# Performance work log

Measured on AMD Instinct MI355X. Metric: run time of the kernel, lower is better.

Reference implementation:

```python
import jax, jax.numpy as jnp
import numpy as np

N, IN_DIM, OUT_DIM = 8192, 512, 256

def setup_inputs() -> dict:
    key = jax.random.key(0)
    k1, k2, k3, k4, k5 = jax.random.split(key, 5)
    feat = jax.random.normal(k1, (N, IN_DIM), dtype=jnp.float32)
    counting_attn = jax.random.uniform(k2, (N, N), dtype=jnp.float32)
    Wq = jax.random.normal(k3, (IN_DIM, OUT_DIM), dtype=jnp.float32) * (IN_DIM ** -0.5)
    Wk = jax.random.normal(k4, (IN_DIM, OUT_DIM), dtype=jnp.float32) * (IN_DIM ** -0.5)
    Wv = jax.random.normal(k5, (IN_DIM, OUT_DIM), dtype=jnp.float32) * (IN_DIM ** -0.5)
    return {"feat": feat, "counting_attn": counting_attn, "Wq": Wq, "Wk": Wk, "Wv": Wv}

def reference(feat, counting_attn, Wq, Wk, Wv):
    # eval mode: feat_drop / attn_drop are identity
    Q = feat @ Wq  # [N, D]
    K = feat @ Wk
    V = feat @ Wv
    scale = 1.0 / jnp.sqrt(jnp.float32(Q.shape[1]))
    logits = (Q @ K.T) * scale  # [N, N]
    logits = logits - jnp.max(logits, axis=1, keepdims=True)
    a_nomi = jnp.exp(logits) * counting_attn
    a_deno = jnp.sum(a_nomi, axis=1, keepdims=True)
    a_nor = a_nomi / (a_deno + 1e-9)
    ret = a_nor @ V  # [N, D]
    return jax.nn.elu(ret)
```

## Files before the change

### kernel.cpp

```cpp
#include <hip/hip_runtime.h>

typedef unsigned short u16;
typedef unsigned int u32;
typedef __attribute__((ext_vector_type(8))) __bf16 bf16x8;
typedef __attribute__((ext_vector_type(16))) float f32x16;

#define NN 8192
#define IND 512
#define DD 256
#define LN_K 0.00195122595f

__device__ __forceinline__ void gl_lds16(const void* g, void* l) {
  __builtin_amdgcn_global_load_lds((const __attribute__((address_space(1))) void*)g,
                                   (__attribute__((address_space(3))) void*)l, 16, 0, 0);
}
__device__ __forceinline__ u16 bf16_rne(float x) {
  u32 u = __float_as_uint(x);
  u += 0x7FFF + ((u >> 16) & 1);
  return (u16)(u >> 16);
}

__global__ __launch_bounds__(256) void wt_transpose(const float* __restrict__ Wq,
                                                    const float* __restrict__ Wk,
                                                    const float* __restrict__ Wv,
                                                    u16* __restrict__ WT) {
  const int o = blockIdx.y;
  const int e = blockIdx.x * 256 + threadIdx.x;
  const int n = e >> 9, k = e & 511;
  const float* W = (o == 0) ? Wq : ((o == 1) ? Wk : Wv);
  WT[o * (DD * IND) + e] = bf16_rne(W[k * DD + n]);
}

__global__ __launch_bounds__(256) void cvt_feat(const float* __restrict__ f,
                                                u16* __restrict__ fb) {
  const int i = (blockIdx.x * 256 + threadIdx.x) * 4;
  float4 v = *(const float4*)(f + i);
  u32 lo = (u32)bf16_rne(v.x) | ((u32)bf16_rne(v.y) << 16);
  u32 hi = (u32)bf16_rne(v.z) | ((u32)bf16_rne(v.w) << 16);
  *(uint2*)(fb + i) = make_uint2(lo, hi);
}

__global__ __launch_bounds__(256, 2) void proj_qkv(const u16* __restrict__ featb,
                                                   const u16* __restrict__ WT,
                                                   u16* __restrict__ Qs,
                                                   u16* __restrict__ Ks,
                                                   u16* __restrict__ VTs) {
  __shared__ u16 tl[4][32 * 40];
  const int mb = blockIdx.x, o = blockIdx.y;
  const int wave = threadIdx.x >> 6, lane = threadIdx.x & 63;
  const int mm = lane & 31, h = lane >> 5;
  const int m0 = mb * 128 + wave * 32;
  const u16* wt = WT + o * (DD * IND);

  f32x16 acc[8];
#pragma unroll
  for (int nt = 0; nt < 8; ++nt)
#pragma unroll
    for (int r = 0; r < 16; ++r) acc[nt][r] = 0.f;

  for (int kc = 0; kc < 32; ++kc) {
    bf16x8 af = *(const bf16x8*)(featb + (size_t)(m0 + mm) * IND + kc * 16 + 8 * h);
#pragma unroll
    for (int nt = 0; nt < 8; ++nt) {
      bf16x8 bf = *(const bf16x8*)(wt + (size_t)(nt * 32 + mm) * IND + kc * 16 + 8 * h);
      acc[nt] = __builtin_amdgcn_mfma_f32_32x32x16_bf16(af, bf, acc[nt], 0, 0, 0);
    }
  }

  if (o < 2) {
    const float sc = (o == 0) ? 0.0625f : 1.f;
    u16* dst = (o == 0) ? Qs : Ks;
#pragma unroll
    for (int nt = 0; nt < 8; ++nt)
#pragma unroll
      for (int r = 0; r < 16; ++r) {
        const int mrow = (r & 3) + 8 * (r >> 2) + 4 * h;
        dst[(size_t)(m0 + mrow) * DD + nt * 32 + mm] = bf16_rne(acc[nt][r] * sc);
      }
  } else {
    const int n2 = lane >> 1, mh = lane & 1;
    for (int nt = 0; nt < 8; ++nt) {
#pragma unroll
      for (int r = 0; r < 16; r += 2) {
        const int mrow = (r & 3) + 8 * (r >> 2) + 4 * h;
        u32 pk = (u32)bf16_rne(acc[nt][r]) | ((u32)bf16_rne(acc[nt][r + 1]) << 16);
        *(u32*)(&tl[wave][mm * 40 + mrow]) = pk;
      }
      __syncthreads();
      bf16x8 t0 = *(const bf16x8*)(&tl[wave][n2 * 40 + mh * 16]);
      bf16x8 t1 = *(const bf16x8*)(&tl[wave][n2 * 40 + mh * 16 + 8]);
      u16* gp = VTs + (size_t)(nt * 32 + n2) * NN + m0 + mh * 16;
      *(bf16x8*)(gp) = t0;
      *(bf16x8*)(gp + 8) = t1;
      __syncthreads();
    }
  }
}

__global__ __launch_bounds__(256, 2) void flash_attn(const u16* __restrict__ Qs,
                                                     const u16* __restrict__ Ks,
                                                     const u16* __restrict__ VTs,
                                                     const float* __restrict__ cnt,
                                                     float* __restrict__ ml,
                                                     float* __restrict__ Op,
                                                     int jiters, int spl) {
  __shared__ u16 kl[2][8192];
  __shared__ u16 vl[2][8192];
  const int bid = blockIdx.x;
  const int lg = __ffs(spl) - 1;
  const int sp = bid & (spl - 1);
  const int rb = bid >> lg;
  const int wave = threadIdx.x >> 6, lane = threadIdx.x & 63;
  const int mm = lane & 31, h = lane >> 5;
  const int m0 = rb * 128 + wave * 32;
  const int jbase = sp * jiters * 32;

  bf16x8 qf[16];
  {
    const u16* qrow = Qs + (size_t)(m0 + mm) * DD;
#pragma unroll
    for (int c = 0; c < 16; ++c) qf[c] = *(const bf16x8*)(qrow + c * 16 + 8 * h);
  }
  f32x16 acc[8];
#pragma unroll
  for (int nt = 0; nt < 8; ++nt)
#pragma unroll
    for (int r = 0; r < 16; ++r) acc[nt][r] = 0.f;
  float m_run = -1e30f, l_run = 0.f;

#pragma unroll
  for (int ii = 0; ii < 4; ++ii) {
    const int w = wave * 4 + ii;
    const int L = w * 64 + lane;
    gl_lds16(Ks + (size_t)(jbase + (L & 31)) * DD + (L >> 5) * 8, (char*)kl + w * 1024);
    gl_lds16(VTs + (size_t)(L & 255) * NN + jbase + (L >> 8) * 8, (char*)vl + w * 1024);
  }

  for (int jb = 0; jb < jiters; ++jb) {
    const int buf = jb & 1;
    const int j0 = jbase + jb * 32;

    float cf[16];
    {
      const float* crow = cnt + (size_t)(m0 + mm) * NN + j0 + 4 * h;
#pragma unroll
      for (int g = 0; g < 4; ++g) {
        float4 t = *(const float4*)(crow + 8 * g);
        cf[4 * g + 0] = t.x;
        cf[4 * g + 1] = t.y;
        cf[4 * g + 2] = t.z;
        cf[4 * g + 3] = t.w;
      }
    }

    asm volatile("s_waitcnt vmcnt(4)" ::: "memory");
    __builtin_amdgcn_s_barrier();
    asm volatile("" ::: "memory");

    if (jb + 1 < jiters) {
      const int jn = j0 + 32;
#pragma unroll
      for (int ii = 0; ii < 4; ++ii) {
        const int w = wave * 4 + ii;
        const int L = w * 64 + lane;
        gl_lds16(Ks + (size_t)(jn + (L & 31)) * DD + (L >> 5) * 8,
                 (char*)kl + (buf ^ 1) * 16384 + w * 1024);
        gl_lds16(VTs + (size_t)(L & 255) * NN + jn + (L >> 8) * 8,
                 (char*)vl + (buf ^ 1) * 16384 + w * 1024);
      }
    }

    const char* klb = (const char*)kl + buf * 16384;
    const char* vlb = (const char*)vl + buf * 16384;
    f32x16 sv0, sv1;
#pragma unroll
    for (int r = 0; r < 16; ++r) { sv0[r] = 0.f; sv1[r] = 0.f; }
    __builtin_amdgcn_s_setprio(1);
#pragma unroll
    for (int c = 0; c < 16; c += 2) {
      bf16x8 kf0 = *(const bf16x8*)(klb + (((2 * c + h) * 32 + mm) << 4));
      bf16x8 kf1 = *(const bf16x8*)(klb + (((2 * c + 2 + h) * 32 + mm) << 4));
      sv0 = __builtin_amdgcn_mfma_f32_32x32x16_bf16(kf0, qf[c], sv0, 0, 0, 0);
      sv1 = __builtin_amdgcn_mfma_f32_32x32x16_bf16(kf1, qf[c + 1], sv1, 0, 0, 0);
    }
    __builtin_amdgcn_s_setprio(0);
    f32x16 sv = sv0 + sv1;

    float mx = sv[0];
#pragma unroll
    for (int r = 1; r < 16; ++r) mx = fmaxf(mx, sv[r]);
    mx = fmaxf(mx, __shfl_xor(mx, 32));
    const float m_new = fmaxf(m_run, mx);
    const bool upd = __any(mx > m_run);
    const float msub = m_new - LN_K;

    float p[16];
    float bsum = 0.f;
#pragma unroll
    for (int r = 0; r < 16; ++r) {
      p[r] = __expf(sv[r] - msub) * cf[r];
      bsum += p[r];
    }
    bsum += __shfl_xor(bsum, 32);

    if (upd) {
      const float alpha = __expf(m_run - m_new);
      l_run = l_run * alpha + bsum;
#pragma unroll
      for (int nt = 0; nt < 8; ++nt)
#pragma unroll
        for (int r = 0; r < 16; ++r) acc[nt][r] *= alpha;
    } else {
      l_run += bsum;
    }
    m_run = m_new;

    u32 P2[8];
#pragma unroll
    for (int j = 0; j < 8; ++j) {
      const u32 ua = __float_as_uint(p[2 * j]);
      const u32 ub = __float_as_uint(p[2 * j + 1]);
      P2[j] = (ua >> 16) | (ub & 0xFFFF0000u);
    }
#pragma unroll
    for (int kc2 = 0; kc2 < 2; ++kc2) {
      union { u32 u[4]; bf16x8 v; } pf;
#pragma unroll
      for (int tp = 0; tp < 4; ++tp) {
        const int src = mm + 32 * (tp >> 1);
        const u32 va = __shfl(P2[4 * kc2 + (tp & 1)], src);
        const u32 vb = __shfl(P2[4 * kc2 + 2 + (tp & 1)], src);
        pf.u[tp] = h ? vb : va;
      }
      __builtin_amdgcn_s_setprio(1);
#pragma unroll
      for (int nt = 0; nt < 8; ++nt) {
        bf16x8 vf = *(const bf16x8*)(vlb + ((((2 * kc2 + h) * 256) + nt * 32 + mm) << 4));
        acc[nt] = __builtin_amdgcn_mfma_f32_32x32x16_bf16(vf, pf.v, acc[nt], 0, 0, 0);
      }
      __builtin_amdgcn_s_setprio(0);
    }
  }

  const int wb = rb * 4 + wave;
  if (lane < 32) {
    ml[((sp * 256 + wb) << 6) + lane] = m_run;
    ml[((sp * 256 + wb) << 6) + 32 + lane] = l_run;
  }
#pragma unroll
  for (int nt = 0; nt < 8; ++nt) {
#pragma unroll
    for (int rr = 0; rr < 4; ++rr) {
      float* op = Op + ((((size_t)(sp * 256 + wb) * 8 + nt) * 4 + rr) * 64 + lane) * 4;
      float4 v = make_float4(acc[nt][4 * rr], acc[nt][4 * rr + 1],
                             acc[nt][4 * rr + 2], acc[nt][4 * rr + 3]);
      *(float4*)op = v;
    }
  }
}

template <int SPL>
__global__ __launch_bounds__(256) void merge_out(const float* __restrict__ ml,
                                                 const float* __restrict__ Op,
                                                 float* __restrict__ out) {
  const int wid = blockIdx.x * 4 + (threadIdx.x >> 6);
  const int lane = threadIdx.x & 63, mm = lane & 31, h = lane >> 5;
  const int wb = wid >> 3, nt = wid & 7;
  float mv[SPL], lv[SPL], wsc[SPL];
#pragma unroll
  for (int s = 0; s < SPL; ++s) {
    mv[s] = ml[((s * 256 + wb) << 6) + mm];
    lv[s] = ml[((s * 256 + wb) << 6) + 32 + mm];
  }
  float M = mv[0];
#pragma unroll
  for (int s = 1; s < SPL; ++s) M = fmaxf(M, mv[s]);
  float L = 0.f;
#pragma unroll
  for (int s = 0; s < SPL; ++s) {
    wsc[s] = __expf(mv[s] - M);
    L += wsc[s] * lv[s];
  }
  const float inv = 1.f / (L + 1e-9f);

  float o[16];
#pragma unroll
  for (int r = 0; r < 16; ++r) o[r] = 0.f;
#pragma unroll
  for (int s = 0; s < SPL; ++s) {
#pragma unroll
    for (int rr = 0; rr < 4; ++rr) {
      const float* op = Op + ((((size_t)(s * 256 + wb) * 8 + nt) * 4 + rr) * 64 + lane) * 4;
      float4 v = *(const float4*)op;
      o[4 * rr + 0] += wsc[s] * v.x;
      o[4 * rr + 1] += wsc[s] * v.y;
      o[4 * rr + 2] += wsc[s] * v.z;
      o[4 * rr + 3] += wsc[s] * v.w;
    }
  }
  const int row = wb * 32 + mm;
#pragma unroll
  for (int g = 0; g < 4; ++g) {
    float4 v;
    float* pv = &v.x;
#pragma unroll
    for (int i = 0; i < 4; ++i) {
      float t = o[4 * g + i] * inv;
      pv[i] = t > 0.f ? t : expm1f(t);
    }
    *(float4*)(out + (size_t)row * DD + nt * 32 + 8 * g + 4 * h) = v;
  }
}

extern "C" void kernel_launch(void* const* d_in, const int* in_sizes, int n_in,
                              void* d_out, int out_size, void* d_ws, size_t ws_size,
                              hipStream_t stream) {
  const float* feat = (const float*)d_in[0];
  const float* cnta = (const float*)d_in[1];
  const float* Wq = (const float*)d_in[2];
  const float* Wk = (const float*)d_in[3];
  const float* Wv = (const float*)d_in[4];
  char* ws = (char*)d_ws;
  u16* WT = (u16*)(ws);
  u16* featb = (u16*)(ws + (1ull << 20));
  u16* Qs = (u16*)(ws + (9ull << 20));
  u16* Ks = (u16*)(ws + (13ull << 20));
  u16* VTs = (u16*)(ws + (17ull << 20));
  float* ml = (float*)(ws + (21ull << 20));
  float* Op = (float*)(ws + (22ull << 20));
  float* out = (float*)d_out;

  const size_t need8 = (22ull << 20) + (64ull << 20);
  const int spl = (ws_size >= need8) ? 8 : 4;
  const int jiters = NN / (spl * 32);

  hipLaunchKernelGGL(wt_transpose, dim3(512, 3), dim3(256), 0, stream, Wq, Wk, Wv, WT);
  hipLaunchKernelGGL(cvt_feat, dim3(4096), dim3(256), 0, stream, feat, featb);
  hipLaunchKernelGGL(proj_qkv, dim3(64, 3), dim3(256), 0, stream, featb, WT, Qs, Ks, VTs);
  hipLaunchKernelGGL(flash_attn, dim3(64 * spl), dim3(256), 0, stream, Qs, Ks, VTs, cnta, ml,
                     Op, jiters, spl);
  if (spl == 8) {
    hipLaunchKernelGGL((merge_out<8>), dim3(512), dim3(256), 0, stream, ml, Op, out);
  } else {
    hipLaunchKernelGGL((merge_out<4>), dim3(512), dim3(256), 0, stream, ml, Op, out);
  }
}
```

Before: 568.1 us.

## Split QKV projection across more blocks, coalesce weight transpose, lazy softmax rescale

The weight transpose now has each thread pack eight bf16 values into one 16-byte store. The QKV projection changes from four waves each computing 32 rows by 256 columns to blocks of 32 rows in which each wave computes 64 columns. That gives four times as many blocks, smaller accumulators and no block-wide barriers. In the attention loop, rescaling of the running max and accumulators now happens only when the new max exceeds the old one by more than 8, which cuts how often the accumulators are rescaled. The trade-off is that exponentials can reach up to e^8 before renormalising. The max and sum reductions are also rewritten as trees to shorten dependency chains.

Result: faster. 546.4 us (-3.8%).

```diff
diff --git a/kernel.cpp b/kernel.cpp
--- a/kernel.cpp
+++ b/kernel.cpp
@@ -25,10 +25,18 @@
                                                     const float* __restrict__ Wv,
                                                     u16* __restrict__ WT) {
   const int o = blockIdx.y;
-  const int e = blockIdx.x * 256 + threadIdx.x;
-  const int n = e >> 9, k = e & 511;
+  const int k0 = blockIdx.x * 8;
+  const int n = threadIdx.x;
   const float* W = (o == 0) ? Wq : ((o == 1) ? Wk : Wv);
-  WT[o * (DD * IND) + e] = bf16_rne(W[k * DD + n]);
+  u32 pk[4];
+#pragma unroll
+  for (int g = 0; g < 4; ++g) {
+    const float a = W[(size_t)(k0 + 2 * g) * DD + n];
+    const float b = W[(size_t)(k0 + 2 * g + 1) * DD + n];
+    pk[g] = (u32)bf16_rne(a) | ((u32)bf16_rne(b) << 16);
+  }
+  *(uint4*)(WT + (size_t)o * (DD * IND) + (size_t)n * IND + k0) =
+      make_uint4(pk[0], pk[1], pk[2], pk[3]);
 }
 
 __global__ __launch_bounds__(256) void cvt_feat(const float* __restrict__ f,
@@ -40,7 +48,7 @@
   *(uint2*)(fb + i) = make_uint2(lo, hi);
 }
 
-__global__ __launch_bounds__(256, 2) void proj_qkv(const u16* __restrict__ featb,
+__global__ __launch_bounds__(256, 4) void proj_qkv(const u16* __restrict__ featb,
                                                    const u16* __restrict__ WT,
                                                    u16* __restrict__ Qs,
                                                    u16* __restrict__ Ks,
@@ -49,21 +57,22 @@
   const int mb = blockIdx.x, o = blockIdx.y;
   const int wave = threadIdx.x >> 6, lane = threadIdx.x & 63;
   const int mm = lane & 31, h = lane >> 5;
-  const int m0 = mb * 128 + wave * 32;
+  const int m0 = mb * 32;
   const u16* wt = WT + o * (DD * IND);
 
-  f32x16 acc[8];
-#pragma unroll
-  for (int nt = 0; nt < 8; ++nt)
-#pragma unroll
-    for (int r = 0; r < 16; ++r) acc[nt][r] = 0.f;
+  f32x16 acc[2];
+#pragma unroll
+  for (int t = 0; t < 2; ++t)
+#pragma unroll
+    for (int r = 0; r < 16; ++r) acc[t][r] = 0.f;
 
   for (int kc = 0; kc < 32; ++kc) {
     bf16x8 af = *(const bf16x8*)(featb + (size_t)(m0 + mm) * IND + kc * 16 + 8 * h);
 #pragma unroll
-    for (int nt = 0; nt < 8; ++nt) {
+    for (int t = 0; t < 2; ++t) {
+      const int nt = wave * 2 + t;
       bf16x8 bf = *(const bf16x8*)(wt + (size_t)(nt * 32 + mm) * IND + kc * 16 + 8 * h);
-      acc[nt] = __builtin_amdgcn_mfma_f32_32x32x16_bf16(af, bf, acc[nt], 0, 0, 0);
+      acc[t] = __builtin_amdgcn_mfma_f32_32x32x16_bf16(af, bf, acc[t], 0, 0, 0);
     }
   }
 
@@ -71,28 +80,30 @@
     const float sc = (o == 0) ? 0.0625f : 1.f;
     u16* dst = (o == 0) ? Qs : Ks;
 #pragma unroll
-    for (int nt = 0; nt < 8; ++nt)
+    for (int t = 0; t < 2; ++t) {
+      const int nt = wave * 2 + t;
 #pragma unroll
       for (int r = 0; r < 16; ++r) {
         const int mrow = (r & 3) + 8 * (r >> 2) + 4 * h;
-        dst[(size_t)(m0 + mrow) * DD + nt * 32 + mm] = bf16_rne(acc[nt][r] * sc);
-      }
+        dst[(size_t)(m0 + mrow) * DD + nt * 32 + mm] = bf16_rne(acc[t][r] * sc);
+      }
+    }
   } else {
     const int n2 = lane >> 1, mh = lane & 1;
-    for (int nt = 0; nt < 8; ++nt) {
+#pragma unroll
+    for (int t = 0; t < 2; ++t) {
+      const int nt = wave * 2 + t;
 #pragma unroll
       for (int r = 0; r < 16; r += 2) {
         const int mrow = (r & 3) + 8 * (r >> 2) + 4 * h;
-        u32 pk = (u32)bf16_rne(acc[nt][r]) | ((u32)bf16_rne(acc[nt][r + 1]) << 16);
+        u32 pk = (u32)bf16_rne(acc[t][r]) | ((u32)bf16_rne(acc[t][r + 1]) << 16);
         *(u32*)(&tl[wave][mm * 40 + mrow]) = pk;
       }
-      __syncthreads();
       bf16x8 t0 = *(const bf16x8*)(&tl[wave][n2 * 40 + mh * 16]);
       bf16x8 t1 = *(const bf16x8*)(&tl[wave][n2 * 40 + mh * 16 + 8]);
       u16* gp = VTs + (size_t)(nt * 32 + n2) * NN + m0 + mh * 16;
       *(bf16x8*)(gp) = t0;
       *(bf16x8*)(gp + 8) = t1;
-      __syncthreads();
     }
   }
 }
@@ -186,34 +197,37 @@
     __builtin_amdgcn_s_setprio(0);
     f32x16 sv = sv0 + sv1;
 
-    float mx = sv[0];
-#pragma unroll
-    for (int r = 1; r < 16; ++r) mx = fmaxf(mx, sv[r]);
+    float ma = fmaxf(fmaxf(sv[0], sv[1]), sv[2]);
+    float mb2 = fmaxf(fmaxf(sv[3], sv[4]), sv[5]);
+    float mc = fmaxf(fmaxf(sv[6], sv[7]), sv[8]);
+    float md = fmaxf(fmaxf(sv[9], sv[10]), sv[11]);
+    float me = fmaxf(fmaxf(sv[12], sv[13]), sv[14]);
+    float mx = fmaxf(fmaxf(fmaxf(ma, mb2), mc), fmaxf(fmaxf(md, me), sv[15]));
     mx = fmaxf(mx, __shfl_xor(mx, 32));
-    const float m_new = fmaxf(m_run, mx);
-    const bool upd = __any(mx > m_run);
-    const float msub = m_new - LN_K;
+
+    const bool upd = __any(mx > m_run + 8.f);
+    if (upd) {
+      const float m_new = fmaxf(m_run, mx);
+      const float alpha = __expf(m_run - m_new);
+      l_run *= alpha;
+#pragma unroll
+      for (int nt = 0; nt < 8; ++nt)
+#pragma unroll
+        for (int r = 0; r < 16; ++r) acc[nt][r] *= alpha;
+      m_run = m_new;
+    }
+    const float msub = m_run - LN_K;
 
     float p[16];
-    float bsum = 0.f;
-#pragma unroll
-    for (int r = 0; r < 16; ++r) {
-      p[r] = __expf(sv[r] - msub) * cf[r];
-      bsum += p[r];
-    }
+#pragma unroll
+    for (int r = 0; r < 16; ++r) p[r] = __expf(sv[r] - msub) * cf[r];
+    float s0 = (p[0] + p[1]) + (p[2] + p[3]);
+    float s1 = (p[4] + p[5]) + (p[6] + p[7]);
+    float s2 = (p[8] + p[9]) + (p[10] + p[11]);
+    float s3 = (p[12] + p[13]) + (p[14] + p[15]);
+    float bsum = (s0 + s1) + (s2 + s3);
     bsum += __shfl_xor(bsum, 32);
-
-    if (upd) {
-      const float alpha = __expf(m_run - m_new);
-      l_run = l_run * alpha + bsum;
-#pragma unroll
-      for (int nt = 0; nt < 8; ++nt)
-#pragma unroll
-        for (int r = 0; r < 16; ++r) acc[nt][r] *= alpha;
-    } else {
-      l_run += bsum;
-    }
-    m_run = m_new;
+    l_run += bsum;
 
     u32 P2[8];
 #pragma unroll
@@ -334,9 +348,9 @@
   const int spl = (ws_size >= need8) ? 8 : 4;
   const int jiters = NN / (spl * 32);
 
-  hipLaunchKernelGGL(wt_transpose, dim3(512, 3), dim3(256), 0, stream, Wq, Wk, Wv, WT);
+  hipLaunchKernelGGL(wt_transpose, dim3(64, 3), dim3(256), 0, stream, Wq, Wk, Wv, WT);
   hipLaunchKernelGGL(cvt_feat, dim3(4096), dim3(256), 0, stream, feat, featb);
-  hipLaunchKernelGGL(proj_qkv, dim3(64, 3), dim3(256), 0, stream, featb, WT, Qs, Ks, VTs);
+  hipLaunchKernelGGL(proj_qkv, dim3(256, 3), dim3(256), 0, stream, featb, WT, Qs, Ks, VTs);
   hipLaunchKernelGGL(flash_attn, dim3(64 * spl), dim3(256), 0, stream, Qs, Ks, VTs, cnta, ml,
                      Op, jiters, spl);
   if (spl == 8) {
```
